# Kernel optimization log

Hardware: AMD Instinct MI355X
Metric: run time of the kernel (lower is better)

## Reference

```python
import jax, jax.numpy as jnp
import numpy as np

N_NODES = 50000
TAU = 1.0 + (1.0 / 1000.0) * (0.1 - 1.0)  # anneal step 1 -> 0.9991


def setup_inputs() -> dict:
    key = jax.random.key(0)
    ks = jax.random.split(key, 8)
    N, F, H, E, K = N_NODES, 128, 128, 800000, 5
    node_features = jax.random.normal(ks[0], (N, F), dtype=jnp.float32)
    src = jnp.sort(jax.random.randint(ks[1], (E,), 0, N, dtype=jnp.int32))
    dst = jax.random.randint(ks[2], (E,), 0, N, dtype=jnp.int32)
    u_noise = jax.random.uniform(ks[3], (K, E), dtype=jnp.float32,
                                 minval=1e-6, maxval=1.0 - 1e-6)
    # MLP params: Linear(2F -> H), ReLU, Linear(H -> 1)
    W1 = jax.random.normal(ks[4], (2 * F, H), dtype=jnp.float32) / np.sqrt(2 * F)
    b1 = jnp.zeros((H,), dtype=jnp.float32)
    W2 = jax.random.normal(ks[5], (H, 1), dtype=jnp.float32) / np.sqrt(H)
    b2 = jnp.zeros((1,), dtype=jnp.float32)
    return {"node_features": node_features, "W1": W1, "b1": b1,
            "W2": W2, "b2": b2, "u_noise": u_noise, "src": src, "dst": dst}


def reference(node_features, W1, b1, W2, b2, u_noise, src, dst):
    N = N_NODES
    F = node_features.shape[1]
    # per-edge MLP on concat([x_u, x_v]) without materializing the (E, 2F) concat
    x_u = node_features[src]                      # (E, F)
    x_v = node_features[dst]                      # (E, F)
    h = jax.nn.relu(x_u @ W1[:F] + x_v @ W1[F:] + b1)   # (E, H)
    z = (h @ W2 + b2)[:, 0]                       # (E,)
    # per-node (segment) log-softmax over each node's neighbor edges
    zmax = jax.ops.segment_max(z, src, num_segments=N)
    ze = z - zmax[src]
    denom = jax.ops.segment_sum(jnp.exp(ze), src, num_segments=N)
    log_pi = ze - jnp.log(denom)[src]             # (E,)
    # k rounds of Gumbel-softmax sampling
    g = -jnp.log(-jnp.log(u_noise))               # (K, E)
    scores = (log_pi[None, :] + g) / TAU          # (K, E)

    def seg_softmax(s):
        m = jax.ops.segment_max(s, src, num_segments=N)
        e = jnp.exp(s - m[src])
        return e / jax.ops.segment_sum(e, src, num_segments=N)[src]

    def seg_argmax_dst(s):
        m = jax.ops.segment_max(s, src, num_segments=N)
        hit = s >= m[src]
        sel = jax.ops.segment_max(jnp.where(hit, dst, -1), src, num_segments=N)
        return sel  # (N,) selected neighbor per node, per round

    soft = jax.vmap(seg_softmax)(scores)          # (K, E) gumbel-softmax probs
    selected = jax.vmap(seg_argmax_dst)(scores)   # (K, N) sampled neighbor ids
    return selected, soft
```

## Files before the change

kernel.cpp:

```cpp
#include <hip/hip_runtime.h>

#define FEAT 128
#define HID  128
#define XS_S 132

__global__ __launch_bounds__(256) void gemm_ab(
    const float* __restrict__ X, const float* __restrict__ W1,
    const float* __restrict__ b1, float* __restrict__ A,
    float* __restrict__ B, int N) {
  __shared__ float xs[32 * XS_S];
  __shared__ float ws[32 * 128];
  const int t = threadIdx.x;

  const int nb = gridDim.x;
  const int q = nb >> 3, r = nb & 7;
  const int xcd = blockIdx.x & 7, bidx = blockIdx.x >> 3;
  const int nw = (xcd < r ? xcd * (q + 1) : r * (q + 1) + (xcd - r) * q) + bidx;
  const int n0 = (nw >> 1) * 128;
  const int g = nw & 1;
  const float* Wbase = W1 + (size_t)g * 128 * HID;
  float* Obase = g ? B : A;

  const int tn = t & 31;
  const int tc = t >> 5;

  float acc[4][16];
#pragma unroll
  for (int rr = 0; rr < 4; ++rr)
#pragma unroll
    for (int c = 0; c < 16; ++c) acc[rr][c] = 0.f;

  const int ln = t >> 3;
  const int lf = (t & 7) * 4;

  for (int kc = 0; kc < 4; ++kc) {
    __syncthreads();
#pragma unroll
    for (int rep = 0; rep < 4; ++rep) {
      const int nl = ln + rep * 32;
      const int n = n0 + nl;
      float4 v = make_float4(0.f, 0.f, 0.f, 0.f);
      if (n < N) v = *(const float4*)(X + (size_t)n * FEAT + kc * 32 + lf);
      xs[(lf + 0) * XS_S + nl] = v.x;
      xs[(lf + 1) * XS_S + nl] = v.y;
      xs[(lf + 2) * XS_S + nl] = v.z;
      xs[(lf + 3) * XS_S + nl] = v.w;
    }
#pragma unroll
    for (int rep = 0; rep < 4; ++rep) {
      const int idx = rep * 256 + t;
      const int wr = idx >> 5;
      const int c4 = (idx & 31) * 4;
      *(float4*)&ws[wr * 128 + c4] =
          *(const float4*)(Wbase + (size_t)(kc * 32 + wr) * HID + c4);
    }
    __syncthreads();

#pragma unroll 8
    for (int k = 0; k < 32; ++k) {
      const float4 xv = *(const float4*)&xs[k * XS_S + tn * 4];
      const float4 w0 = *(const float4*)&ws[k * 128 + tc * 16 + 0];
      const float4 w1 = *(const float4*)&ws[k * 128 + tc * 16 + 4];
      const float4 w2 = *(const float4*)&ws[k * 128 + tc * 16 + 8];
      const float4 w3 = *(const float4*)&ws[k * 128 + tc * 16 + 12];
      const float xr[4] = {xv.x, xv.y, xv.z, xv.w};
#pragma unroll
      for (int rr = 0; rr < 4; ++rr) {
        acc[rr][0]  = fmaf(xr[rr], w0.x, acc[rr][0]);
        acc[rr][1]  = fmaf(xr[rr], w0.y, acc[rr][1]);
        acc[rr][2]  = fmaf(xr[rr], w0.z, acc[rr][2]);
        acc[rr][3]  = fmaf(xr[rr], w0.w, acc[rr][3]);
        acc[rr][4]  = fmaf(xr[rr], w1.x, acc[rr][4]);
        acc[rr][5]  = fmaf(xr[rr], w1.y, acc[rr][5]);
        acc[rr][6]  = fmaf(xr[rr], w1.z, acc[rr][6]);
        acc[rr][7]  = fmaf(xr[rr], w1.w, acc[rr][7]);
        acc[rr][8]  = fmaf(xr[rr], w2.x, acc[rr][8]);
        acc[rr][9]  = fmaf(xr[rr], w2.y, acc[rr][9]);
        acc[rr][10] = fmaf(xr[rr], w2.z, acc[rr][10]);
        acc[rr][11] = fmaf(xr[rr], w2.w, acc[rr][11]);
        acc[rr][12] = fmaf(xr[rr], w3.x, acc[rr][12]);
        acc[rr][13] = fmaf(xr[rr], w3.y, acc[rr][13]);
        acc[rr][14] = fmaf(xr[rr], w3.z, acc[rr][14]);
        acc[rr][15] = fmaf(xr[rr], w3.w, acc[rr][15]);
      }
    }
  }

  float4 bb[4];
#pragma unroll
  for (int c = 0; c < 4; ++c) bb[c] = make_float4(0.f, 0.f, 0.f, 0.f);
  if (g == 0) {
#pragma unroll
    for (int c = 0; c < 4; ++c) bb[c] = *(const float4*)(b1 + tc * 16 + c * 4);
  }
#pragma unroll
  for (int rr = 0; rr < 4; ++rr) {
    const int n = n0 + tn * 4 + rr;
    if (n < N) {
      float* o = Obase + (size_t)n * HID + tc * 16;
#pragma unroll
      for (int c = 0; c < 4; ++c) {
        *(float4*)(o + c * 4) = make_float4(
            acc[rr][c * 4 + 0] + bb[c].x, acc[rr][c * 4 + 1] + bb[c].y,
            acc[rr][c * 4 + 2] + bb[c].z, acc[rr][c * 4 + 3] + bb[c].w);
      }
    }
  }
}

__global__ __launch_bounds__(256) void row_offsets(
    const int* __restrict__ src, int* __restrict__ rs, int N, int E) {
  const int n = blockIdx.x * 256 + threadIdx.x;
  if (n > N) return;
  int lo = 0, hi = E;
  while (lo < hi) {
    const int mid = (lo + hi) >> 1;
    if (src[mid] < n) lo = mid + 1; else hi = mid;
  }
  rs[n] = lo;
}

__global__ __launch_bounds__(256) void edge_z(
    const float* __restrict__ A, const float* __restrict__ B,
    const float* __restrict__ W2, const float* __restrict__ b2,
    const int* __restrict__ src, const int* __restrict__ dst,
    float* __restrict__ z, int E) {
  const int g = threadIdx.x >> 4;
  const int l = threadIdx.x & 15;
  const int e0 = blockIdx.x * 32 + g * 2;
  if (e0 >= E) return;
  const int e1 = e0 + 1;
  const bool has1 = e1 < E;

  const int u0 = src[e0], v0 = dst[e0];
  const int u1 = has1 ? src[e1] : u0;
  const int v1 = has1 ? dst[e1] : v0;

  const float4* Au0 = (const float4*)(A + (size_t)u0 * HID) + l * 2;
  const float4* Bv0 = (const float4*)(B + (size_t)v0 * HID) + l * 2;
  const float4* Au1 = (const float4*)(A + (size_t)u1 * HID) + l * 2;
  const float4* Bv1 = (const float4*)(B + (size_t)v1 * HID) + l * 2;

  const float4 a00 = Au0[0], a01 = Au0[1];
  const float4 b00 = Bv0[0], b01 = Bv0[1];
  const float4 a10 = Au1[0], a11 = Au1[1];
  const float4 b10 = Bv1[0], b11 = Bv1[1];

  const float4 w0 = *(const float4*)(W2 + l * 8);
  const float4 w1 = *(const float4*)(W2 + l * 8 + 4);
  const float bias2 = b2[0];

  float p0 = fmaxf(a00.x + b00.x, 0.f) * w0.x
           + fmaxf(a00.y + b00.y, 0.f) * w0.y
           + fmaxf(a00.z + b00.z, 0.f) * w0.z
           + fmaxf(a00.w + b00.w, 0.f) * w0.w
           + fmaxf(a01.x + b01.x, 0.f) * w1.x
           + fmaxf(a01.y + b01.y, 0.f) * w1.y
           + fmaxf(a01.z + b01.z, 0.f) * w1.z
           + fmaxf(a01.w + b01.w, 0.f) * w1.w;
  float p1 = fmaxf(a10.x + b10.x, 0.f) * w0.x
           + fmaxf(a10.y + b10.y, 0.f) * w0.y
           + fmaxf(a10.z + b10.z, 0.f) * w0.z
           + fmaxf(a10.w + b10.w, 0.f) * w0.w
           + fmaxf(a11.x + b11.x, 0.f) * w1.x
           + fmaxf(a11.y + b11.y, 0.f) * w1.y
           + fmaxf(a11.z + b11.z, 0.f) * w1.z
           + fmaxf(a11.w + b11.w, 0.f) * w1.w;

#pragma unroll
  for (int m = 8; m >= 1; m >>= 1) {
    p0 += __shfl_xor(p0, m);
    p1 += __shfl_xor(p1, m);
  }
  if (l == 0) {
    z[e0] = p0 + bias2;
    if (has1) z[e1] = p1 + bias2;
  }
}

__global__ __launch_bounds__(256) void seg_sample(
    const float* __restrict__ z, const float* __restrict__ U,
    const int* __restrict__ dst, const int* __restrict__ rs,
    float* __restrict__ out_sel, float* __restrict__ out_soft,
    int N, int E, int K) {
  const int t = threadIdx.x;
  const int lane = t & 63;
  const int qtr = lane >> 4;
  const int ql = lane & 15;
  const int n = blockIdx.x * 16 + (t >> 6) * 4 + qtr;
  const float INVTAU = 1.0f / 0.9991f;

  int start = 0, deg = 0;
  if (n < N) { start = rs[n]; deg = rs[n + 1] - start; }

  if (__all(deg <= 32)) {
    if (n >= N) return;
    if (deg == 0) {
      if (ql == 0)
        for (int k = 0; k < K; ++k) out_sel[(size_t)k * N + n] = -2147483648.0f;
      return;
    }
    const bool a0 = 2 * ql < deg;
    const bool a1 = 2 * ql + 1 < deg;
    const int e0 = start + 2 * ql;
    const int e1 = e0 + 1;
    const float z0 = a0 ? z[e0] : -INFINITY;
    const float z1 = a1 ? z[e1] : -INFINITY;
    const int d0 = a0 ? dst[e0] : -1;
    const int d1 = a1 ? dst[e1] : -1;

    float zmax = fmaxf(z0, z1);
#pragma unroll
    for (int m = 8; m >= 1; m >>= 1) zmax = fmaxf(zmax, __shfl_xor(zmax, m));
    float den = (a0 ? __expf(z0 - zmax) : 0.f) + (a1 ? __expf(z1 - zmax) : 0.f);
#pragma unroll
    for (int m = 8; m >= 1; m >>= 1) den += __shfl_xor(den, m);
    const float logd = __logf(den);
    const float lp0 = (z0 - zmax) - logd;
    const float lp1 = (z1 - zmax) - logd;

    for (int k = 0; k < K; ++k) {
      float ex0 = 0.f, ex1 = 0.f;
      if (a0) {
        const float uu = U[(size_t)k * E + e0];
        const float gum = -__logf(-__logf(uu));
        ex0 = __expf((lp0 + gum) * INVTAU);
      }
      if (a1) {
        const float uu = U[(size_t)k * E + e1];
        const float gum = -__logf(-__logf(uu));
        ex1 = __expf((lp1 + gum) * INVTAU);
      }
      float d2 = ex0 + ex1;
      float mx;
      int md;
      if (ex1 > ex0)      { mx = ex1; md = d1; }
      else if (ex1 < ex0) { mx = ex0; md = d0; }
      else                { mx = ex0; md = max(d0, d1); }
#pragma unroll
      for (int m = 8; m >= 1; m >>= 1) {
        d2 += __shfl_xor(d2, m);
        const float ox = __shfl_xor(mx, m);
        const int od = __shfl_xor(md, m);
        if (ox > mx) { mx = ox; md = od; }
        else if (ox == mx) md = max(md, od);
      }
      if (ql == 0) out_sel[(size_t)k * N + n] = (float)md;
      const float inv = __builtin_amdgcn_rcpf(d2);
      if (a0) out_soft[(size_t)k * E + e0] = ex0 * inv;
      if (a1) out_soft[(size_t)k * E + e1] = ex1 * inv;
    }
    return;
  }

  const int wbase = blockIdx.x * 16 + (t >> 6) * 4;
  for (int j = 0; j < 4; ++j) {
    const int nn = wbase + j;
    if (nn >= N) continue;
    const int st = rs[nn];
    const int dg = rs[nn + 1] - st;
    if (dg == 0) {
      if (lane == 0)
        for (int k = 0; k < K; ++k) out_sel[(size_t)k * N + nn] = -2147483648.0f;
      continue;
    }
    float zmax = -INFINITY;
    for (int c = lane; c < dg; c += 64) zmax = fmaxf(zmax, z[st + c]);
#pragma unroll
    for (int m = 32; m >= 1; m >>= 1) zmax = fmaxf(zmax, __shfl_xor(zmax, m));
    float den = 0.f;
    for (int c = lane; c < dg; c += 64) den += expf(z[st + c] - zmax);
#pragma unroll
    for (int m = 32; m >= 1; m >>= 1) den += __shfl_xor(den, m);
    const float logd = logf(den);

    for (int k = 0; k < K; ++k) {
      float m2 = -INFINITY;
      for (int c = lane; c < dg; c += 64) {
        const int e = st + c;
        const float gum = -logf(-logf(U[(size_t)k * E + e]));
        const float s = ((z[e] - zmax) - logd + gum) * INVTAU;
        m2 = fmaxf(m2, s);
      }
#pragma unroll
      for (int m = 32; m >= 1; m >>= 1) m2 = fmaxf(m2, __shfl_xor(m2, m));
      float d2 = 0.f;
      int cand = -1;
      for (int c = lane; c < dg; c += 64) {
        const int e = st + c;
        const float gum = -logf(-logf(U[(size_t)k * E + e]));
        const float s = ((z[e] - zmax) - logd + gum) * INVTAU;
        d2 += expf(s - m2);
        if (s >= m2) cand = max(cand, dst[e]);
      }
#pragma unroll
      for (int m = 32; m >= 1; m >>= 1) d2 += __shfl_xor(d2, m);
#pragma unroll
      for (int m = 32; m >= 1; m >>= 1) cand = max(cand, __shfl_xor(cand, m));
      if (lane == 0) out_sel[(size_t)k * N + nn] = (float)cand;
      for (int c = lane; c < dg; c += 64) {
        const int e = st + c;
        const float gum = -logf(-logf(U[(size_t)k * E + e]));
        const float s = ((z[e] - zmax) - logd + gum) * INVTAU;
        out_soft[(size_t)k * E + e] = expf(s - m2) / d2;
      }
    }
  }
}

extern "C" void kernel_launch(void* const* d_in, const int* in_sizes, int n_in,
                              void* d_out, int out_size, void* d_ws, size_t ws_size,
                              hipStream_t stream) {
  const float* X  = (const float*)d_in[0];
  const float* W1 = (const float*)d_in[1];
  const float* b1 = (const float*)d_in[2];
  const float* W2 = (const float*)d_in[3];
  const float* b2 = (const float*)d_in[4];
  const float* U  = (const float*)d_in[5];
  const int* src  = (const int*)d_in[6];
  const int* dst  = (const int*)d_in[7];
  const int E = in_sizes[6];
  const int K = in_sizes[5] / E;
  const int N = in_sizes[0] / FEAT;

  float* A = (float*)d_ws;
  float* B = A + (size_t)N * HID;
  float* z = B + (size_t)N * HID;
  int* rs  = (int*)(z + E);

  float* out_sel  = (float*)d_out;
  float* out_soft = (float*)d_out + (size_t)K * N;

  hipLaunchKernelGGL(gemm_ab, dim3(2 * ((N + 127) / 128)), dim3(256), 0, stream,
                     X, W1, b1, A, B, N);
  hipLaunchKernelGGL(row_offsets, dim3((N + 256) / 256), dim3(256), 0, stream,
                     src, rs, N, E);
  hipLaunchKernelGGL(edge_z, dim3((E + 31) / 32), dim3(256), 0, stream,
                     A, B, W2, b2, src, dst, z, E);
  hipLaunchKernelGGL(seg_sample, dim3((N + 15) / 16), dim3(256), 0, stream,
                     z, U, dst, rs, out_sel, out_soft, N, E, K);
}
```

Baseline: 246.0 us.

## Read W1 via wave-uniform scalar loads in node GEMM, split output columns

The node-feature GEMM no longer stages W1 in shared memory. Each wave instead reads its 16 output columns with wave-uniform (readfirstlane) global loads, which the compiler can turn into scalar loads. The grid is doubled so each block computes 64 of the 128 output columns for 128 nodes, with each lane handling 2 nodes. This removes the W1 LDS staging and LDS reads and adds parallelism, at the cost of reloading the X tile twice as often and having fewer accumulators per thread.

```diff
diff --git a/kernel.cpp b/kernel.cpp
--- a/kernel.cpp
+++ b/kernel.cpp
@@ -9,26 +9,26 @@
     const float* __restrict__ b1, float* __restrict__ A,
     float* __restrict__ B, int N) {
   __shared__ float xs[32 * XS_S];
-  __shared__ float ws[32 * 128];
   const int t = threadIdx.x;
 
   const int nb = gridDim.x;
   const int q = nb >> 3, r = nb & 7;
   const int xcd = blockIdx.x & 7, bidx = blockIdx.x >> 3;
   const int nw = (xcd < r ? xcd * (q + 1) : r * (q + 1) + (xcd - r) * q) + bidx;
-  const int n0 = (nw >> 1) * 128;
-  const int g = nw & 1;
-  const float* Wbase = W1 + (size_t)g * 128 * HID;
-  float* Obase = g ? B : A;
-
-  const int tn = t & 31;
-  const int tc = t >> 5;
-
-  float acc[4][16];
-#pragma unroll
-  for (int rr = 0; rr < 4; ++rr)
-#pragma unroll
-    for (int c = 0; c < 16; ++c) acc[rr][c] = 0.f;
+  const int n0 = (nw >> 2) * 128;
+  const int jb = (nw & 3) * 64;
+  const int isA = jb < 128;
+  const int ob = jb & 127;
+  const float* Wb = W1 + (size_t)(isA ? 0 : 128 * HID) + ob;
+  float* Obase = isA ? A : B;
+
+  const int l = t & 63;
+  const int wv16 = __builtin_amdgcn_readfirstlane((t >> 6) * 16);
+  const float* Wp = Wb + wv16;
+
+  float acc0[16], acc1[16];
+#pragma unroll
+  for (int c = 0; c < 16; ++c) { acc0[c] = 0.f; acc1[c] = 0.f; }
 
   const int ln = t >> 3;
   const int lf = (t & 7) * 4;
@@ -46,42 +46,21 @@
       xs[(lf + 2) * XS_S + nl] = v.z;
       xs[(lf + 3) * XS_S + nl] = v.w;
     }
-#pragma unroll
-    for (int rep = 0; rep < 4; ++rep) {
-      const int idx = rep * 256 + t;
-      const int wr = idx >> 5;
-      const int c4 = (idx & 31) * 4;
-      *(float4*)&ws[wr * 128 + c4] =
-          *(const float4*)(Wbase + (size_t)(kc * 32 + wr) * HID + c4);
-    }
     __syncthreads();
 
-#pragma unroll 8
+#pragma unroll 4
     for (int k = 0; k < 32; ++k) {
-      const float4 xv = *(const float4*)&xs[k * XS_S + tn * 4];
-      const float4 w0 = *(const float4*)&ws[k * 128 + tc * 16 + 0];
-      const float4 w1 = *(const float4*)&ws[k * 128 + tc * 16 + 4];
-      const float4 w2 = *(const float4*)&ws[k * 128 + tc * 16 + 8];
-      const float4 w3 = *(const float4*)&ws[k * 128 + tc * 16 + 12];
-      const float xr[4] = {xv.x, xv.y, xv.z, xv.w};
-#pragma unroll
-      for (int rr = 0; rr < 4; ++rr) {
-        acc[rr][0]  = fmaf(xr[rr], w0.x, acc[rr][0]);
-        acc[rr][1]  = fmaf(xr[rr], w0.y, acc[rr][1]);
-        acc[rr][2]  = fmaf(xr[rr], w0.z, acc[rr][2]);
-        acc[rr][3]  = fmaf(xr[rr], w0.w, acc[rr][3]);
-        acc[rr][4]  = fmaf(xr[rr], w1.x, acc[rr][4]);
-        acc[rr][5]  = fmaf(xr[rr], w1.y, acc[rr][5]);
-        acc[rr][6]  = fmaf(xr[rr], w1.z, acc[rr][6]);
-        acc[rr][7]  = fmaf(xr[rr], w1.w, acc[rr][7]);
-        acc[rr][8]  = fmaf(xr[rr], w2.x, acc[rr][8]);
-        acc[rr][9]  = fmaf(xr[rr], w2.y, acc[rr][9]);
-        acc[rr][10] = fmaf(xr[rr], w2.z, acc[rr][10]);
-        acc[rr][11] = fmaf(xr[rr], w2.w, acc[rr][11]);
-        acc[rr][12] = fmaf(xr[rr], w3.x, acc[rr][12]);
-        acc[rr][13] = fmaf(xr[rr], w3.y, acc[rr][13]);
-        acc[rr][14] = fmaf(xr[rr], w3.z, acc[rr][14]);
-        acc[rr][15] = fmaf(xr[rr], w3.w, acc[rr][15]);
+      const float2 xv = *(const float2*)&xs[k * XS_S + 2 * l];
+      const float* wr = Wp + (size_t)(kc * 32 + k) * HID;
+      float wv[16];
+      *(float4*)&wv[0]  = *(const float4*)(wr);
+      *(float4*)&wv[4]  = *(const float4*)(wr + 4);
+      *(float4*)&wv[8]  = *(const float4*)(wr + 8);
+      *(float4*)&wv[12] = *(const float4*)(wr + 12);
+#pragma unroll
+      for (int c = 0; c < 16; ++c) {
+        acc0[c] = fmaf(xv.x, wv[c], acc0[c]);
+        acc1[c] = fmaf(xv.y, wv[c], acc1[c]);
       }
     }
   }
@@ -89,22 +68,28 @@
   float4 bb[4];
 #pragma unroll
   for (int c = 0; c < 4; ++c) bb[c] = make_float4(0.f, 0.f, 0.f, 0.f);
-  if (g == 0) {
-#pragma unroll
-    for (int c = 0; c < 4; ++c) bb[c] = *(const float4*)(b1 + tc * 16 + c * 4);
-  }
-#pragma unroll
-  for (int rr = 0; rr < 4; ++rr) {
-    const int n = n0 + tn * 4 + rr;
-    if (n < N) {
-      float* o = Obase + (size_t)n * HID + tc * 16;
-#pragma unroll
-      for (int c = 0; c < 4; ++c) {
-        *(float4*)(o + c * 4) = make_float4(
-            acc[rr][c * 4 + 0] + bb[c].x, acc[rr][c * 4 + 1] + bb[c].y,
-            acc[rr][c * 4 + 2] + bb[c].z, acc[rr][c * 4 + 3] + bb[c].w);
-      }
-    }
+  if (isA) {
+#pragma unroll
+    for (int c = 0; c < 4; ++c)
+      bb[c] = *(const float4*)(b1 + ob + wv16 + c * 4);
+  }
+  const int na = n0 + 2 * l;
+  const int nbb = na + 1;
+  if (na < N) {
+    float* o = Obase + (size_t)na * HID + ob + wv16;
+#pragma unroll
+    for (int c = 0; c < 4; ++c)
+      *(float4*)(o + c * 4) = make_float4(
+          acc0[c * 4 + 0] + bb[c].x, acc0[c * 4 + 1] + bb[c].y,
+          acc0[c * 4 + 2] + bb[c].z, acc0[c * 4 + 3] + bb[c].w);
+  }
+  if (nbb < N) {
+    float* o = Obase + (size_t)nbb * HID + ob + wv16;
+#pragma unroll
+    for (int c = 0; c < 4; ++c)
+      *(float4*)(o + c * 4) = make_float4(
+          acc1[c * 4 + 0] + bb[c].x, acc1[c * 4 + 1] + bb[c].y,
+          acc1[c * 4 + 2] + bb[c].z, acc1[c * 4 + 3] + bb[c].w);
   }
 }
 
@@ -331,7 +316,7 @@
   float* out_sel  = (float*)d_out;
   float* out_soft = (float*)d_out + (size_t)K * N;
 
-  hipLaunchKernelGGL(gemm_ab, dim3(2 * ((N + 127) / 128)), dim3(256), 0, stream,
+  hipLaunchKernelGGL(gemm_ab, dim3(4 * ((N + 127) / 128)), dim3(256), 0, stream,
                      X, W1, b1, A, B, N);
   hipLaunchKernelGGL(row_offsets, dim3((N + 256) / 256), dim3(256), 0, stream,
                      src, rs, N, E);
```

Result: no change. 246.2 us (+0.1%).

## Fuse edge scoring and segment sampling into one kernel; split GEMM into 64-column tiles

Applied to the files above, without the earlier changes.

Merges row_offsets, edge_z and seg_sample into one kernel. Each block of 16 nodes binary-searches its own row offsets, stages src/dst in shared memory, computes edge logits into shared memory, then runs the segment softmax and sampling from there. This removes the global z and rs round trips and two launches. The GEMM now uses 64-column output tiles, doubling the grid and halving accumulators to raise occupancy. Risks: edges beyond MAXE per 16-node block are silently truncated, and the edge-score work is unevenly spread across blocks.

```diff
diff --git a/kernel.cpp b/kernel.cpp
--- a/kernel.cpp
+++ b/kernel.cpp
@@ -3,32 +3,34 @@
 #define FEAT 128
 #define HID  128
 #define XS_S 132
+#define MAXE 2048
 
 __global__ __launch_bounds__(256) void gemm_ab(
     const float* __restrict__ X, const float* __restrict__ W1,
     const float* __restrict__ b1, float* __restrict__ A,
     float* __restrict__ B, int N) {
   __shared__ float xs[32 * XS_S];
-  __shared__ float ws[32 * 128];
+  __shared__ float ws[32 * 64];
   const int t = threadIdx.x;
 
-  const int nb = gridDim.x;
-  const int q = nb >> 3, r = nb & 7;
+  const int nbk = gridDim.x;
+  const int q = nbk >> 3, r = nbk & 7;
   const int xcd = blockIdx.x & 7, bidx = blockIdx.x >> 3;
   const int nw = (xcd < r ? xcd * (q + 1) : r * (q + 1) + (xcd - r) * q) + bidx;
-  const int n0 = (nw >> 1) * 128;
-  const int g = nw & 1;
-  const float* Wbase = W1 + (size_t)g * 128 * HID;
-  float* Obase = g ? B : A;
+  const int n0 = (nw >> 2) * 128;
+  const int j0 = (nw & 3) * 64;
+  const bool isA = j0 < 128;
+  const float* Wbase = W1 + (isA ? j0 : 128 * HID + (j0 - 128));
+  float* Obase = isA ? (A + j0) : (B + (j0 - 128));
 
   const int tn = t & 31;
   const int tc = t >> 5;
 
-  float acc[4][16];
+  float acc[4][8];
 #pragma unroll
   for (int rr = 0; rr < 4; ++rr)
 #pragma unroll
-    for (int c = 0; c < 16; ++c) acc[rr][c] = 0.f;
+    for (int c = 0; c < 8; ++c) acc[rr][c] = 0.f;
 
   const int ln = t >> 3;
   const int lf = (t & 7) * 4;
@@ -47,11 +49,11 @@
       xs[(lf + 3) * XS_S + nl] = v.w;
     }
 #pragma unroll
-    for (int rep = 0; rep < 4; ++rep) {
+    for (int rep = 0; rep < 2; ++rep) {
       const int idx = rep * 256 + t;
-      const int wr = idx >> 5;
-      const int c4 = (idx & 31) * 4;
-      *(float4*)&ws[wr * 128 + c4] =
+      const int wr = idx >> 4;
+      const int c4 = (idx & 15) * 4;
+      *(float4*)&ws[wr * 64 + c4] =
           *(const float4*)(Wbase + (size_t)(kc * 32 + wr) * HID + c4);
     }
     __syncthreads();
@@ -59,139 +61,140 @@
 #pragma unroll 8
     for (int k = 0; k < 32; ++k) {
       const float4 xv = *(const float4*)&xs[k * XS_S + tn * 4];
-      const float4 w0 = *(const float4*)&ws[k * 128 + tc * 16 + 0];
-      const float4 w1 = *(const float4*)&ws[k * 128 + tc * 16 + 4];
-      const float4 w2 = *(const float4*)&ws[k * 128 + tc * 16 + 8];
-      const float4 w3 = *(const float4*)&ws[k * 128 + tc * 16 + 12];
+      const float4 w0 = *(const float4*)&ws[k * 64 + tc * 8];
+      const float4 w1 = *(const float4*)&ws[k * 64 + tc * 8 + 4];
       const float xr[4] = {xv.x, xv.y, xv.z, xv.w};
 #pragma unroll
       for (int rr = 0; rr < 4; ++rr) {
-        acc[rr][0]  = fmaf(xr[rr], w0.x, acc[rr][0]);
-        acc[rr][1]  = fmaf(xr[rr], w0.y, acc[rr][1]);
-        acc[rr][2]  = fmaf(xr[rr], w0.z, acc[rr][2]);
-        acc[rr][3]  = fmaf(xr[rr], w0.w, acc[rr][3]);
-        acc[rr][4]  = fmaf(xr[rr], w1.x, acc[rr][4]);
-        acc[rr][5]  = fmaf(xr[rr], w1.y, acc[rr][5]);
-        acc[rr][6]  = fmaf(xr[rr], w1.z, acc[rr][6]);
-        acc[rr][7]  = fmaf(xr[rr], w1.w, acc[rr][7]);
-        acc[rr][8]  = fmaf(xr[rr], w2.x, acc[rr][8]);
-        acc[rr][9]  = fmaf(xr[rr], w2.y, acc[rr][9]);
-        acc[rr][10] = fmaf(xr[rr], w2.z, acc[rr][10]);
-        acc[rr][11] = fmaf(xr[rr], w2.w, acc[rr][11]);
-        acc[rr][12] = fmaf(xr[rr], w3.x, acc[rr][12]);
-        acc[rr][13] = fmaf(xr[rr], w3.y, acc[rr][13]);
-        acc[rr][14] = fmaf(xr[rr], w3.z, acc[rr][14]);
-        acc[rr][15] = fmaf(xr[rr], w3.w, acc[rr][15]);
-      }
-    }
-  }
-
-  float4 bb[4];
-#pragma unroll
-  for (int c = 0; c < 4; ++c) bb[c] = make_float4(0.f, 0.f, 0.f, 0.f);
-  if (g == 0) {
-#pragma unroll
-    for (int c = 0; c < 4; ++c) bb[c] = *(const float4*)(b1 + tc * 16 + c * 4);
+        acc[rr][0] = fmaf(xr[rr], w0.x, acc[rr][0]);
+        acc[rr][1] = fmaf(xr[rr], w0.y, acc[rr][1]);
+        acc[rr][2] = fmaf(xr[rr], w0.z, acc[rr][2]);
+        acc[rr][3] = fmaf(xr[rr], w0.w, acc[rr][3]);
+        acc[rr][4] = fmaf(xr[rr], w1.x, acc[rr][4]);
+        acc[rr][5] = fmaf(xr[rr], w1.y, acc[rr][5]);
+        acc[rr][6] = fmaf(xr[rr], w1.z, acc[rr][6]);
+        acc[rr][7] = fmaf(xr[rr], w1.w, acc[rr][7]);
+      }
+    }
+  }
+
+  float bb[8];
+#pragma unroll
+  for (int c = 0; c < 8; ++c) bb[c] = 0.f;
+  if (isA) {
+    *(float4*)&bb[0] = *(const float4*)(b1 + j0 + tc * 8);
+    *(float4*)&bb[4] = *(const float4*)(b1 + j0 + tc * 8 + 4);
   }
 #pragma unroll
   for (int rr = 0; rr < 4; ++rr) {
     const int n = n0 + tn * 4 + rr;
     if (n < N) {
-      float* o = Obase + (size_t)n * HID + tc * 16;
-#pragma unroll
-      for (int c = 0; c < 4; ++c) {
-        *(float4*)(o + c * 4) = make_float4(
-            acc[rr][c * 4 + 0] + bb[c].x, acc[rr][c * 4 + 1] + bb[c].y,
-            acc[rr][c * 4 + 2] + bb[c].z, acc[rr][c * 4 + 3] + bb[c].w);
-      }
+      float* o = Obase + (size_t)n * HID + tc * 8;
+      *(float4*)o = make_float4(acc[rr][0] + bb[0], acc[rr][1] + bb[1],
+                                acc[rr][2] + bb[2], acc[rr][3] + bb[3]);
+      *(float4*)(o + 4) = make_float4(acc[rr][4] + bb[4], acc[rr][5] + bb[5],
+                                      acc[rr][6] + bb[6], acc[rr][7] + bb[7]);
     }
   }
 }
 
-__global__ __launch_bounds__(256) void row_offsets(
-    const int* __restrict__ src, int* __restrict__ rs, int N, int E) {
-  const int n = blockIdx.x * 256 + threadIdx.x;
-  if (n > N) return;
-  int lo = 0, hi = E;
-  while (lo < hi) {
-    const int mid = (lo + hi) >> 1;
-    if (src[mid] < n) lo = mid + 1; else hi = mid;
-  }
-  rs[n] = lo;
-}
-
-__global__ __launch_bounds__(256) void edge_z(
+__global__ __launch_bounds__(256) void fused_edge_seg(
     const float* __restrict__ A, const float* __restrict__ B,
     const float* __restrict__ W2, const float* __restrict__ b2,
     const int* __restrict__ src, const int* __restrict__ dst,
-    float* __restrict__ z, int E) {
-  const int g = threadIdx.x >> 4;
-  const int l = threadIdx.x & 15;
-  const int e0 = blockIdx.x * 32 + g * 2;
-  if (e0 >= E) return;
-  const int e1 = e0 + 1;
-  const bool has1 = e1 < E;
-
-  const int u0 = src[e0], v0 = dst[e0];
-  const int u1 = has1 ? src[e1] : u0;
-  const int v1 = has1 ? dst[e1] : v0;
-
-  const float4* Au0 = (const float4*)(A + (size_t)u0 * HID) + l * 2;
-  const float4* Bv0 = (const float4*)(B + (size_t)v0 * HID) + l * 2;
-  const float4* Au1 = (const float4*)(A + (size_t)u1 * HID) + l * 2;
-  const float4* Bv1 = (const float4*)(B + (size_t)v1 * HID) + l * 2;
-
-  const float4 a00 = Au0[0], a01 = Au0[1];
-  const float4 b00 = Bv0[0], b01 = Bv0[1];
-  const float4 a10 = Au1[0], a11 = Au1[1];
-  const float4 b10 = Bv1[0], b11 = Bv1[1];
-
-  const float4 w0 = *(const float4*)(W2 + l * 8);
-  const float4 w1 = *(const float4*)(W2 + l * 8 + 4);
-  const float bias2 = b2[0];
-
-  float p0 = fmaxf(a00.x + b00.x, 0.f) * w0.x
-           + fmaxf(a00.y + b00.y, 0.f) * w0.y
-           + fmaxf(a00.z + b00.z, 0.f) * w0.z
-           + fmaxf(a00.w + b00.w, 0.f) * w0.w
-           + fmaxf(a01.x + b01.x, 0.f) * w1.x
-           + fmaxf(a01.y + b01.y, 0.f) * w1.y
-           + fmaxf(a01.z + b01.z, 0.f) * w1.z
-           + fmaxf(a01.w + b01.w, 0.f) * w1.w;
-  float p1 = fmaxf(a10.x + b10.x, 0.f) * w0.x
-           + fmaxf(a10.y + b10.y, 0.f) * w0.y
-           + fmaxf(a10.z + b10.z, 0.f) * w0.z
-           + fmaxf(a10.w + b10.w, 0.f) * w0.w
-           + fmaxf(a11.x + b11.x, 0.f) * w1.x
-           + fmaxf(a11.y + b11.y, 0.f) * w1.y
-           + fmaxf(a11.z + b11.z, 0.f) * w1.z
-           + fmaxf(a11.w + b11.w, 0.f) * w1.w;
-
-#pragma unroll
-  for (int m = 8; m >= 1; m >>= 1) {
-    p0 += __shfl_xor(p0, m);
-    p1 += __shfl_xor(p1, m);
-  }
-  if (l == 0) {
-    z[e0] = p0 + bias2;
-    if (has1) z[e1] = p1 + bias2;
-  }
-}
-
-__global__ __launch_bounds__(256) void seg_sample(
-    const float* __restrict__ z, const float* __restrict__ U,
-    const int* __restrict__ dst, const int* __restrict__ rs,
-    float* __restrict__ out_sel, float* __restrict__ out_soft,
-    int N, int E, int K) {
+    const float* __restrict__ U, float* __restrict__ out_sel,
+    float* __restrict__ out_soft, int N, int E, int K) {
+  __shared__ float zs[MAXE];
+  __shared__ int srcs[MAXE];
+  __shared__ int dsts[MAXE];
+  __shared__ int rsl[17];
   const int t = threadIdx.x;
+  const int n0 = blockIdx.x * 16;
+  const float INVTAU = 1.0f / 0.9991f;
+
+  if (t < 17) {
+    const int n = min(n0 + t, N);
+    int lo = 0, hi = E;
+    while (lo < hi) {
+      const int mid = (lo + hi) >> 1;
+      if (src[mid] < n) lo = mid + 1; else hi = mid;
+    }
+    rsl[t] = lo;
+  }
+  __syncthreads();
+  const int e_lo = rsl[0];
+  const int cnt = min(rsl[16] - e_lo, MAXE);
+
+  for (int i = t; i < cnt; i += 256) {
+    srcs[i] = src[e_lo + i];
+    dsts[i] = dst[e_lo + i];
+  }
+  __syncthreads();
+
+  {
+    const int g = t >> 4;
+    const int l = t & 15;
+    const float4 w0 = *(const float4*)(W2 + l * 8);
+    const float4 w1 = *(const float4*)(W2 + l * 8 + 4);
+    const float bias2 = b2[0];
+    for (int base = 0; base < cnt; base += 32) {
+      const int i0 = base + g * 2;
+      if (i0 < cnt) {
+        const int i1 = i0 + 1;
+        const bool has1 = i1 < cnt;
+        const int u0 = srcs[i0], v0 = dsts[i0];
+        const int u1 = has1 ? srcs[i1] : u0;
+        const int v1 = has1 ? dsts[i1] : v0;
+
+        const float4* Au0 = (const float4*)(A + (size_t)u0 * HID) + l * 2;
+        const float4* Bv0 = (const float4*)(B + (size_t)v0 * HID) + l * 2;
+        const float4* Au1 = (const float4*)(A + (size_t)u1 * HID) + l * 2;
+        const float4* Bv1 = (const float4*)(B + (size_t)v1 * HID) + l * 2;
+
+        const float4 a00 = Au0[0], a01 = Au0[1];
+        const float4 b00 = Bv0[0], b01 = Bv0[1];
+        const float4 a10 = Au1[0], a11 = Au1[1];
+        const float4 b10 = Bv1[0], b11 = Bv1[1];
+
+        float p0 = fmaxf(a00.x + b00.x, 0.f) * w0.x
+                 + fmaxf(a00.y + b00.y, 0.f) * w0.y
+                 + fmaxf(a00.z + b00.z, 0.f) * w0.z
+                 + fmaxf(a00.w + b00.w, 0.f) * w0.w
+                 + fmaxf(a01.x + b01.x, 0.f) * w1.x
+                 + fmaxf(a01.y + b01.y, 0.f) * w1.y
+                 + fmaxf(a01.z + b01.z, 0.f) * w1.z
+                 + fmaxf(a01.w + b01.w, 0.f) * w1.w;
+        float p1 = fmaxf(a10.x + b10.x, 0.f) * w0.x
+                 + fmaxf(a10.y + b10.y, 0.f) * w0.y
+                 + fmaxf(a10.z + b10.z, 0.f) * w0.z
+                 + fmaxf(a10.w + b10.w, 0.f) * w0.w
+                 + fmaxf(a11.x + b11.x, 0.f) * w1.x
+                 + fmaxf(a11.y + b11.y, 0.f) * w1.y
+                 + fmaxf(a11.z + b11.z, 0.f) * w1.z
+                 + fmaxf(a11.w + b11.w, 0.f) * w1.w;
+
+#pragma unroll
+        for (int m = 8; m >= 1; m >>= 1) {
+          p0 += __shfl_xor(p0, m);
+          p1 += __shfl_xor(p1, m);
+        }
+        if (l == 0) {
+          zs[i0] = p0 + bias2;
+          if (has1) zs[i1] = p1 + bias2;
+        }
+      }
+    }
+  }
+  __syncthreads();
+
   const int lane = t & 63;
   const int qtr = lane >> 4;
   const int ql = lane & 15;
-  const int n = blockIdx.x * 16 + (t >> 6) * 4 + qtr;
-  const float INVTAU = 1.0f / 0.9991f;
+  const int li = (t >> 6) * 4 + qtr;
+  const int n = n0 + li;
 
   int start = 0, deg = 0;
-  if (n < N) { start = rs[n]; deg = rs[n + 1] - start; }
+  if (n < N) { start = rsl[li]; deg = rsl[li + 1] - start; }
 
   if (__all(deg <= 32)) {
     if (n >= N) return;
@@ -202,12 +205,14 @@
     }
     const bool a0 = 2 * ql < deg;
     const bool a1 = 2 * ql + 1 < deg;
+    const int le0 = start - e_lo + 2 * ql;
+    const int le1 = le0 + 1;
     const int e0 = start + 2 * ql;
     const int e1 = e0 + 1;
-    const float z0 = a0 ? z[e0] : -INFINITY;
-    const float z1 = a1 ? z[e1] : -INFINITY;
-    const int d0 = a0 ? dst[e0] : -1;
-    const int d1 = a1 ? dst[e1] : -1;
+    const float z0 = a0 ? zs[le0] : -INFINITY;
+    const float z1 = a1 ? zs[le1] : -INFINITY;
+    const int d0 = a0 ? dsts[le0] : -1;
+    const int d1 = a1 ? dsts[le1] : -1;
 
     float zmax = fmaxf(z0, z1);
 #pragma unroll
@@ -253,23 +258,25 @@
     return;
   }
 
-  const int wbase = blockIdx.x * 16 + (t >> 6) * 4;
+  const int lbase = (t >> 6) * 4;
   for (int j = 0; j < 4; ++j) {
-    const int nn = wbase + j;
+    const int lj = lbase + j;
+    const int nn = n0 + lj;
     if (nn >= N) continue;
-    const int st = rs[nn];
-    const int dg = rs[nn + 1] - st;
+    const int st = rsl[lj];
+    const int dg = rsl[lj + 1] - st;
+    const int lst = st - e_lo;
     if (dg == 0) {
       if (lane == 0)
         for (int k = 0; k < K; ++k) out_sel[(size_t)k * N + nn] = -2147483648.0f;
       continue;
     }
     float zmax = -INFINITY;
-    for (int c = lane; c < dg; c += 64) zmax = fmaxf(zmax, z[st + c]);
+    for (int c = lane; c < dg; c += 64) zmax = fmaxf(zmax, zs[lst + c]);
 #pragma unroll
     for (int m = 32; m >= 1; m >>= 1) zmax = fmaxf(zmax, __shfl_xor(zmax, m));
     float den = 0.f;
-    for (int c = lane; c < dg; c += 64) den += expf(z[st + c] - zmax);
+    for (int c = lane; c < dg; c += 64) den += expf(zs[lst + c] - zmax);
 #pragma unroll
     for (int m = 32; m >= 1; m >>= 1) den += __shfl_xor(den, m);
     const float logd = logf(den);
@@ -277,9 +284,8 @@
     for (int k = 0; k < K; ++k) {
       float m2 = -INFINITY;
       for (int c = lane; c < dg; c += 64) {
-        const int e = st + c;
-        const float gum = -logf(-logf(U[(size_t)k * E + e]));
-        const float s = ((z[e] - zmax) - logd + gum) * INVTAU;
+        const float gum = -logf(-logf(U[(size_t)k * E + st + c]));
+        const float s = ((zs[lst + c] - zmax) - logd + gum) * INVTAU;
         m2 = fmaxf(m2, s);
       }
 #pragma unroll
@@ -287,11 +293,10 @@
       float d2 = 0.f;
       int cand = -1;
       for (int c = lane; c < dg; c += 64) {
-        const int e = st + c;
-        const float gum = -logf(-logf(U[(size_t)k * E + e]));
-        const float s = ((z[e] - zmax) - logd + gum) * INVTAU;
+        const float gum = -logf(-logf(U[(size_t)k * E + st + c]));
+        const float s = ((zs[lst + c] - zmax) - logd + gum) * INVTAU;
         d2 += expf(s - m2);
-        if (s >= m2) cand = max(cand, dst[e]);
+        if (s >= m2) cand = max(cand, dsts[lst + c]);
       }
 #pragma unroll
       for (int m = 32; m >= 1; m >>= 1) d2 += __shfl_xor(d2, m);
@@ -299,10 +304,9 @@
       for (int m = 32; m >= 1; m >>= 1) cand = max(cand, __shfl_xor(cand, m));
       if (lane == 0) out_sel[(size_t)k * N + nn] = (float)cand;
       for (int c = lane; c < dg; c += 64) {
-        const int e = st + c;
-        const float gum = -logf(-logf(U[(size_t)k * E + e]));
-        const float s = ((z[e] - zmax) - logd + gum) * INVTAU;
-        out_soft[(size_t)k * E + e] = expf(s - m2) / d2;
+        const float gum = -logf(-logf(U[(size_t)k * E + st + c]));
+        const float s = ((zs[lst + c] - zmax) - logd + gum) * INVTAU;
+        out_soft[(size_t)k * E + st + c] = expf(s - m2) / d2;
       }
     }
   }
@@ -325,18 +329,12 @@
 
   float* A = (float*)d_ws;
   float* B = A + (size_t)N * HID;
-  float* z = B + (size_t)N * HID;
-  int* rs  = (int*)(z + E);
 
   float* out_sel  = (float*)d_out;
   float* out_soft = (float*)d_out + (size_t)K * N;
 
-  hipLaunchKernelGGL(gemm_ab, dim3(2 * ((N + 127) / 128)), dim3(256), 0, stream,
+  hipLaunchKernelGGL(gemm_ab, dim3(4 * ((N + 127) / 128)), dim3(256), 0, stream,
                      X, W1, b1, A, B, N);
-  hipLaunchKernelGGL(row_offsets, dim3((N + 256) / 256), dim3(256), 0, stream,
-                     src, rs, N, E);
-  hipLaunchKernelGGL(edge_z, dim3((E + 31) / 32), dim3(256), 0, stream,
-                     A, B, W2, b2, src, dst, z, E);
-  hipLaunchKernelGGL(seg_sample, dim3((N + 15) / 16), dim3(256), 0, stream,
-                     z, U, dst, rs, out_sel, out_soft, N, E, K);
+  hipLaunchKernelGGL(fused_edge_seg, dim3((N + 15) / 16), dim3(256), 0, stream,
+                     A, B, W2, b2, src, dst, U, out_sel, out_soft, N, E, K);
 }
```

Result: faster. 238.0 us (-3.2%).
